# Optimization experiments

Hardware: AMD Instinct MI355X
Metric: run time of the kernel (lower is better)

Reference implementation:

```python
import jax, jax.numpy as jnp
import numpy as np

N = 100000
E = 1200000
IN_DIM, PE_DIM, HID, LAT, K = 48, 16, 64, 32, 4


def setup_inputs() -> dict:
    key = jax.random.key(0)
    ks = jax.random.split(key, 12)
    s = 0.05
    return {
        "x": jax.random.normal(ks[0], (N, IN_DIM), dtype=jnp.float32),
        "edge_index": jax.random.randint(ks[1], (2, E), 0, N, dtype=jnp.int32),
        "lap_pe": jax.random.normal(ks[2], (N, PE_DIM), dtype=jnp.float32),
        "cheb1_W": jax.random.normal(ks[3], (K, IN_DIM + PE_DIM, HID), dtype=jnp.float32) * s,
        "cheb1_b": jnp.zeros((HID,), dtype=jnp.float32),
        "cheb2_W": jax.random.normal(ks[4], (K, HID, HID), dtype=jnp.float32) * s,
        "cheb2_b": jnp.zeros((HID,), dtype=jnp.float32),
        "mu_W": jax.random.normal(ks[5], (HID, LAT), dtype=jnp.float32) * s,
        "mu_b": jnp.zeros((LAT,), dtype=jnp.float32),
        "lv_W": jax.random.normal(ks[6], (HID, LAT), dtype=jnp.float32) * s,
        "lv_b": jnp.zeros((LAT,), dtype=jnp.float32),
    }


def _cheb_norm(edge_index, num_nodes):
    # PyG ChebConv.__norm__ with edge_weight=ones (self-loops added then removed),
    # normalization='sym', lambda_max=2.0. Scaled Laplacian L_hat = L - I has
    # zero diagonal and off-diagonal -D^{-1/2} A D^{-1/2}.
    row, col = edge_index[0], edge_index[1]
    w = jnp.where(row == col, 0.0, 1.0).astype(jnp.float32)  # remove_self_loops
    deg = jax.ops.segment_sum(w, row, num_segments=num_nodes)
    dis = jnp.where(deg > 0, jax.lax.rsqrt(jnp.maximum(deg, 1.0)), 0.0)
    norm = -dis[row] * w * dis[col]  # (2/lambda_max)=1 with lambda_max=2
    return row, col, norm


def _cheb_conv(x, row, col, norm, W, b):
    num_nodes = x.shape[0]

    def prop(h):  # L_hat @ h : gather sources, scale, scatter to targets
        return jax.ops.segment_sum(norm[:, None] * h[row], col, num_segments=num_nodes)

    Tx0 = x
    out = Tx0 @ W[0]
    Tx1 = prop(Tx0)
    out = out + Tx1 @ W[1]
    for k in range(2, W.shape[0]):  # Chebyshev recurrence T_k = 2 L T_{k-1} - T_{k-2}
        Tx2 = 2.0 * prop(Tx1) - Tx0
        out = out + Tx2 @ W[k]
        Tx0, Tx1 = Tx1, Tx2
    return out + b


def reference(x, edge_index, lap_pe, cheb1_W, cheb1_b, cheb2_W, cheb2_b, mu_W, mu_b, lv_W, lv_b):
    num_nodes = x.shape[0]
    xc = jnp.concatenate([x, lap_pe], axis=1)  # [N, in+pe]
    # forward adds self-loops (weight 1) but ChebConv strips them again internally
    row, col, norm = _cheb_norm(edge_index, num_nodes)
    h = jax.nn.relu(_cheb_conv(xc, row, col, norm, cheb1_W, cheb1_b))
    h = jax.nn.relu(_cheb_conv(h, row, col, norm, cheb2_W, cheb2_b))
    graph_embed = jnp.mean(h, axis=0, keepdims=True)  # scatter_mean, batch all-zero -> [1, HID]
    mu = graph_embed @ mu_W + mu_b
    logvar = graph_embed @ lv_W + lv_b
    return mu, logvar
```

## Files before the change

kernel.cpp:

```cpp
#include <hip/hip_runtime.h>


#define WPB 4
#define CAP 48
#define EB  256

typedef unsigned int u32;
typedef unsigned short u16;
typedef __bf16 bf16x8 __attribute__((ext_vector_type(8)));
typedef float f32x4 __attribute__((ext_vector_type(4)));

__device__ __forceinline__ float bf2f(u16 h) { return __uint_as_float(((u32)h) << 16); }
__device__ __forceinline__ u16 f2bf(float f) {
  u32 u = __float_as_uint(f);
  return (u16)((u + 0x7fffu + ((u >> 16) & 1u)) >> 16);
}
__device__ __forceinline__ u32 cvtpk_bf16(float lo, float hi) {
  u32 r;
  asm("v_cvt_pk_bf16_f32 %0, %1, %2" : "=v"(r) : "v"(lo), "v"(hi));
  return r;
}
__device__ __forceinline__ u32 pk_fp8x4(float a, float b, float c, float d) {
  u32 r = __builtin_amdgcn_cvt_pk_fp8_f32(a, b, 0u, false);
  return __builtin_amdgcn_cvt_pk_fp8_f32(c, d, r, true);
}


__global__ void __launch_bounds__(256) k_b1(const int* __restrict__ ei, int E, int EPB,
                                            int NBC, u32* __restrict__ H) {
  __shared__ u32 sh[2048];
  int nbt = 2 * NBC;
  for (int i = threadIdx.x; i < nbt; i += 256) sh[i] = 0;
  __syncthreads();
  int s = blockIdx.x * EPB, e1 = s + EPB;
  if (e1 > E) e1 = E;
  for (int e = s + threadIdx.x; e < e1; e += 256) {
    int r = ei[e], c = ei[E + e];
    if (r == c) continue;
    atomicAdd(&sh[c >> 7], 1u);
    atomicAdd(&sh[NBC + (r >> 7)], 1u);
  }
  __syncthreads();
  for (int i = threadIdx.x; i < nbt; i += 256) H[(size_t)i * EB + blockIdx.x] = sh[i];
}

__global__ void __launch_bounds__(256) k_b2a(const u32* __restrict__ H, u32* __restrict__ P,
                                             u32* __restrict__ S) {
  __shared__ u32 sh[EB];
  int bb = blockIdx.x, tid = threadIdx.x;
  u32 v = H[(size_t)bb * EB + tid];
  sh[tid] = v;
  __syncthreads();
  for (int ofs = 1; ofs < EB; ofs <<= 1) {
    u32 add = (tid >= ofs) ? sh[tid - ofs] : 0;
    __syncthreads();
    sh[tid] += add;
    __syncthreads();
  }
  P[(size_t)bb * EB + tid] = sh[tid] - v;
  if (tid == EB - 1) S[bb] = sh[EB - 1];
}

__global__ void __launch_bounds__(256) k_b3(const int* __restrict__ ei, int E, int EPB,
                                            int NBC, const u32* __restrict__ P,
                                            const u32* __restrict__ S,
                                            u32* __restrict__ BaseOut,
                                            u32* __restrict__ cbuf) {
  __shared__ u32 cur[2048];
  __shared__ u32 sh2[256];
  int nbt = 2 * NBC, tid = threadIdx.x;
  int per = (nbt + 255) / 256;
  u32 loc = 0;
  for (int i = 0; i < per; i++) {
    int idx = tid * per + i;
    if (idx < nbt) loc += S[idx];
  }
  sh2[tid] = loc;
  __syncthreads();
  for (int ofs = 1; ofs < 256; ofs <<= 1) {
    u32 a = (tid >= ofs) ? sh2[tid - ofs] : 0;
    __syncthreads();
    sh2[tid] += a;
    __syncthreads();
  }
  u32 run = sh2[tid] - loc;
  for (int i = 0; i < per; i++) {
    int idx = tid * per + i;
    if (idx < nbt) {
      cur[idx] = run + P[(size_t)idx * EB + blockIdx.x];
      if (blockIdx.x == 0) BaseOut[idx] = run;
      run += S[idx];
    }
  }
  if (blockIdx.x == 0 && tid == 255) BaseOut[nbt] = run;
  __syncthreads();
  int s = blockIdx.x * EPB, e1 = s + EPB;
  if (e1 > E) e1 = E;
  for (int e = s + tid; e < e1; e += 256) {
    int r = ei[e], c = ei[E + e];
    if (r == c) continue;
    u32 p1 = atomicAdd(&cur[c >> 7], 1u);
    cbuf[p1] = ((u32)r << 7) | (u32)(c & 127);
    u32 p2 = atomicAdd(&cur[NBC + (r >> 7)], 1u);
    cbuf[p2] = (u32)(r & 127);
  }
}

__global__ void __launch_bounds__(256) k_b4(const u32* __restrict__ Base, int NBC, int N,
                                            const u32* __restrict__ cbuf,
                                            int* __restrict__ csr, int* __restrict__ cnt,
                                            int* __restrict__ deg) {
  __shared__ u32 h[128];
  int bb = blockIdx.x, tid = threadIdx.x;
  if (tid < 128) h[tid] = 0;
  __syncthreads();
  u32 lo = Base[bb], hi = Base[bb + 1];
  if (bb < NBC) {
    int c0 = bb << 7;
    for (u32 e = lo + tid; e < hi; e += 256) {
      u32 w = cbuf[e];
      int cl = w & 127;
      u32 p = atomicAdd(&h[cl], 1u);
      if (p < CAP) csr[(size_t)(c0 + cl) * CAP + p] = (int)(w >> 7);
    }
    __syncthreads();
    if (tid < 128 && c0 + tid < N) cnt[c0 + tid] = (int)h[tid];
  } else {
    int r0 = (bb - NBC) << 7;
    for (u32 e = lo + tid; e < hi; e += 256) atomicAdd(&h[cbuf[e] & 127], 1u);
    __syncthreads();
    if (tid < 128 && r0 + tid < N) deg[r0 + tid] = (int)h[tid];
  }
}


__global__ void k_dis(const int* __restrict__ deg, float2* __restrict__ dis2, int N) {
  int v = blockIdx.x * blockDim.x + threadIdx.x;
  if (v < N) {
    int d = deg[v];
    float df = (float)d;
    dis2[v] = (d > 0) ? make_float2(rsqrtf(df), sqrtf(df)) : make_float2(0.f, 0.f);
  }
}

__global__ void k_init(const float* __restrict__ W1, const float* __restrict__ W2,
                       u16* __restrict__ Wt1, u16* __restrict__ Wt2,
                       u32* g0, u32* g1, u32* g2, u32* g3, int N) {
  int b = blockIdx.x;
  if (b < 128) {
    const float* W = (b < 64) ? W1 : W2;
    u16* Wt = (b < 64) ? Wt1 : Wt2;
    int i = (b & 63) * 256 + threadIdx.x;
    int k = i >> 6, c = i & 63;
    Wt[c * 256 + k] = f2bf(W[i]);
  } else if (threadIdx.x < 64) {
    int tid = threadIdx.x;
    u32* p = (tid < 16) ? g0 : (tid < 32) ? g1 : (tid < 48) ? g2 : g3;
    p[(size_t)N * 16 + (tid & 15)] = 0;
  }
}

__global__ void __launch_bounds__(256) k_concat(
    const float* __restrict__ x, const float* __restrict__ pe,
    const float2* __restrict__ dis2,
    u16* __restrict__ T0, u32* __restrict__ G0, int N) {
  __shared__ float tl[WPB][64];
  int tid = threadIdx.x, lane = tid & 63, wv = tid >> 6;
  int v = blockIdx.x * WPB + wv;
  if (v >= N) return;
  float t = (lane < 48) ? x[(size_t)v * 48 + lane] : pe[(size_t)v * 16 + (lane - 48)];
  T0[(size_t)v * 64 + lane] = f2bf(t);
  tl[wv][lane] = dis2[v].x * t;
  if (lane < 16) {
    const float* p = &tl[wv][lane * 4];
    G0[(size_t)v * 16 + lane] = pk_fp8x4(p[0], p[1], p[2], p[3]);
  }
}

template <int SUB>
__global__ void __launch_bounds__(256) k_prop(
    const int* __restrict__ cnt, const int* __restrict__ csr,
    const float2* __restrict__ dis2,
    const u32* __restrict__ Gsrc, const u32* __restrict__ Gsub,
    u32* __restrict__ Gdst, int N) {
  int tid = threadIdx.x, lane = tid & 63, wv = tid >> 6;
  int half = lane >> 5, sl = lane & 31;
  int v = (blockIdx.x * WPB + wv) * 2 + half;
  int vc = v < N ? v : N - 1;
  int c = (v < N) ? cnt[vc] : 0;
  if (c > CAP) c = CAP;
  const int* base = csr + (size_t)vc * CAP;
  int u0 = (sl < c) ? base[sl] : N;
  int u1 = N;
  if (c > 32 && sl < 16) {
    int s2 = 32 + sl;
    u1 = (s2 < c) ? base[s2] : N;
  }
  int g = (lane >> 3) & 3, fq = lane & 7;
  int sbase = half << 5;
  float a0 = 0, a1 = 0, a2 = 0, a3 = 0, a4 = 0, a5 = 0, a6 = 0, a7 = 0;
#define PGRP(UU, i) { int u = __shfl(UU, sbase + (((i) << 2) | g)); \
    uint2 q = *(const uint2*)(Gsrc + (size_t)u * 16 + fq * 2); \
    auto l0 = __builtin_amdgcn_cvt_pk_f32_fp8(q.x, false); \
    auto h0 = __builtin_amdgcn_cvt_pk_f32_fp8(q.x, true); \
    auto l1 = __builtin_amdgcn_cvt_pk_f32_fp8(q.y, false); \
    auto h1 = __builtin_amdgcn_cvt_pk_f32_fp8(q.y, true); \
    a0 += l0[0]; a1 += l0[1]; a2 += h0[0]; a3 += h0[1]; \
    a4 += l1[0]; a5 += l1[1]; a6 += h1[0]; a7 += h1[1]; }
  PGRP(u0, 0) PGRP(u0, 1) PGRP(u0, 2) PGRP(u0, 3)
  if (c > 16) { PGRP(u0, 4) PGRP(u0, 5) PGRP(u0, 6) PGRP(u0, 7) }
  if (c > 32) { PGRP(u1, 0) PGRP(u1, 1) PGRP(u1, 2) PGRP(u1, 3) }
#undef PGRP
  a0 += __shfl_xor(a0, 8); a0 += __shfl_xor(a0, 16);
  a1 += __shfl_xor(a1, 8); a1 += __shfl_xor(a1, 16);
  a2 += __shfl_xor(a2, 8); a2 += __shfl_xor(a2, 16);
  a3 += __shfl_xor(a3, 8); a3 += __shfl_xor(a3, 16);
  a4 += __shfl_xor(a4, 8); a4 += __shfl_xor(a4, 16);
  a5 += __shfl_xor(a5, 8); a5 += __shfl_xor(a5, 16);
  a6 += __shfl_xor(a6, 8); a6 += __shfl_xor(a6, 16);
  a7 += __shfl_xor(a7, 8); a7 += __shfl_xor(a7, 16);
  if (sl < 8 && v < N) {
    float2 dd = dis2[v];
    float t0 = -dd.x * a0, t1 = -dd.x * a1, t2 = -dd.x * a2, t3 = -dd.x * a3;
    float t4 = -dd.x * a4, t5 = -dd.x * a5, t6 = -dd.x * a6, t7 = -dd.x * a7;
    if (SUB) {
      uint2 sq = *(const uint2*)(Gsub + (size_t)v * 16 + fq * 2);
      auto l0 = __builtin_amdgcn_cvt_pk_f32_fp8(sq.x, false);
      auto h0 = __builtin_amdgcn_cvt_pk_f32_fp8(sq.x, true);
      auto l1 = __builtin_amdgcn_cvt_pk_f32_fp8(sq.y, false);
      auto h1 = __builtin_amdgcn_cvt_pk_f32_fp8(sq.y, true);
      t0 = 2.f * t0 - dd.y * l0[0];
      t1 = 2.f * t1 - dd.y * l0[1];
      t2 = 2.f * t2 - dd.y * h0[0];
      t3 = 2.f * t3 - dd.y * h0[1];
      t4 = 2.f * t4 - dd.y * l1[0];
      t5 = 2.f * t5 - dd.y * l1[1];
      t6 = 2.f * t6 - dd.y * h1[0];
      t7 = 2.f * t7 - dd.y * h1[1];
    }
    uint2 o;
    o.x = pk_fp8x4(dd.x * t0, dd.x * t1, dd.x * t2, dd.x * t3);
    o.y = pk_fp8x4(dd.x * t4, dd.x * t5, dd.x * t6, dd.x * t7);
    *(uint2*)(Gdst + (size_t)v * 16 + fq * 2) = o;
  }
}

__device__ __forceinline__ bf16x8 fp8_frag(const u32* rp, float s) {
  u32 q0 = rp[0], q1 = rp[1];
  auto a = __builtin_amdgcn_cvt_pk_f32_fp8(q0, false);
  auto b = __builtin_amdgcn_cvt_pk_f32_fp8(q0, true);
  auto c = __builtin_amdgcn_cvt_pk_f32_fp8(q1, false);
  auto d = __builtin_amdgcn_cvt_pk_f32_fp8(q1, true);
  union { u32 q[4]; bf16x8 v; } r;
  r.q[0] = cvtpk_bf16(a[0] * s, a[1] * s);
  r.q[1] = cvtpk_bf16(b[0] * s, b[1] * s);
  r.q[2] = cvtpk_bf16(c[0] * s, c[1] * s);
  r.q[3] = cvtpk_bf16(d[0] * s, d[1] * s);
  return r.v;
}

template <int EPI>
__global__ void __launch_bounds__(256) k_gemm(
    const u16* __restrict__ T, const u32* __restrict__ G0,
    const u32* __restrict__ G1, const u32* __restrict__ G2,
    const u32* __restrict__ G3,
    const u16* __restrict__ Wt, const float* __restrict__ bias,
    const float2* __restrict__ dis2,
    u32* __restrict__ outG, float* __restrict__ gm, int N) {
  __shared__ float smem[EPI ? 256 : 4 * 16 * 65];
  int tid = threadIdx.x, lane = tid & 63, wv = tid >> 6;
  int r0 = blockIdx.x * 64 + wv * 16;
  int fr = lane & 15, kg = lane >> 4;
  int arow = r0 + fr;
  if (arow > N - 1) arow = N - 1;
  float dvi = dis2[arow].y;
  f32x4 acc[4] = {};
  const u16* wb = Wt + (size_t)fr * 256 + kg * 8;
  const u32* gbuf[4] = {G0, G1, G2, G3};
#pragma unroll
  for (int s = 0; s < 8; ++s) {
    bf16x8 a;
    if (EPI == 0 && s < 2)
      a = *(const bf16x8*)(T + (size_t)arow * 64 + s * 32 + kg * 8);
    else
      a = fp8_frag(gbuf[s >> 1] + (size_t)arow * 16 + (s & 1) * 8 + kg * 2, dvi);
#pragma unroll
    for (int cc = 0; cc < 4; ++cc) {
      bf16x8 b = *(const bf16x8*)(wb + (size_t)cc * 16 * 256 + s * 32);
      acc[cc] = __builtin_amdgcn_mfma_f32_16x16x32_bf16(a, b, acc[cc], 0, 0, 0);
    }
  }
  if (EPI == 0) {
    float* hl = smem + wv * 16 * 65;
#pragma unroll
    for (int reg = 0; reg < 4; ++reg) {
#pragma unroll
      for (int cc = 0; cc < 4; ++cc) {
        float vv = acc[cc][reg] + bias[cc * 16 + fr];
        hl[(kg * 4 + reg) * 65 + cc * 16 + fr] = vv > 0.f ? vv : 0.f;
      }
    }
    int rr = lane >> 2, dg = lane & 3;
    int grow = r0 + rr;
    if (grow < N) {
      float ds = dis2[grow].x;
      const float* hp = hl + rr * 65 + dg * 16;
      uint4 o;
      o.x = pk_fp8x4(ds * hp[0], ds * hp[1], ds * hp[2], ds * hp[3]);
      o.y = pk_fp8x4(ds * hp[4], ds * hp[5], ds * hp[6], ds * hp[7]);
      o.z = pk_fp8x4(ds * hp[8], ds * hp[9], ds * hp[10], ds * hp[11]);
      o.w = pk_fp8x4(ds * hp[12], ds * hp[13], ds * hp[14], ds * hp[15]);
      *(uint4*)(outG + (size_t)grow * 16 + dg * 4) = o;
    }
  } else {
    float pc[4] = {0.f, 0.f, 0.f, 0.f};
#pragma unroll
    for (int reg = 0; reg < 4; ++reg) {
      int row = r0 + kg * 4 + reg;
      if (row < N) {
#pragma unroll
        for (int cc = 0; cc < 4; ++cc) {
          float vv = acc[cc][reg] + bias[cc * 16 + fr];
          pc[cc] += (vv > 0.f ? vv : 0.f);
        }
      }
    }
#pragma unroll
    for (int cc = 0; cc < 4; ++cc) {
      pc[cc] += __shfl_xor(pc[cc], 16);
      pc[cc] += __shfl_xor(pc[cc], 32);
    }
    if (lane < 16) {
#pragma unroll
      for (int cc = 0; cc < 4; ++cc) smem[wv * 64 + cc * 16 + lane] = pc[cc];
    }
    __syncthreads();
    if (tid < 64)
      atomicAdd(&gm[(blockIdx.x & 63) * 64 + tid],
                smem[tid] + smem[64 + tid] + smem[128 + tid] + smem[192 + tid]);
  }
}

__global__ void k_head(const float* __restrict__ gm, int N,
                       const float* __restrict__ muW, const float* __restrict__ mub,
                       const float* __restrict__ lvW, const float* __restrict__ lvb,
                       float* __restrict__ outp) {
  __shared__ float gs[64];
  int j = threadIdx.x;
  if (j < 64) {
    float s = 0.f;
    for (int k = 0; k < 64; ++k) s += gm[k * 64 + j];
    gs[j] = s;
  }
  __syncthreads();
  if (j < 64) {
    const float* W = (j < 32) ? muW : lvW;
    const float* b = (j < 32) ? mub : lvb;
    int jj = j & 31;
    float invN = 1.0f / (float)N;
    float acc = 0.0f;
    for (int f = 0; f < 64; f++) acc = fmaf(gs[f] * invN, W[f * 32 + jj], acc);
    outp[j] = acc + b[jj];
  }
}

extern "C" void kernel_launch(void* const* d_in, const int* in_sizes, int n_in,
                              void* d_out, int out_size, void* d_ws, size_t ws_size,
                              hipStream_t stream) {
  const float* x   = (const float*)d_in[0];
  const int*   ei  = (const int*)d_in[1];
  const float* pe  = (const float*)d_in[2];
  const float* W1  = (const float*)d_in[3];
  const float* b1  = (const float*)d_in[4];
  const float* W2  = (const float*)d_in[5];
  const float* b2  = (const float*)d_in[6];
  const float* muW = (const float*)d_in[7];
  const float* mub = (const float*)d_in[8];
  const float* lvW = (const float*)d_in[9];
  const float* lvb = (const float*)d_in[10];
  const int N = in_sizes[0] / 48;
  const int E = in_sizes[1] / 2;
  const int NBC = (N + 127) >> 7;
  const int NBT = 2 * NBC;
  const int EPB = (E + EB - 1) / EB;

  char* ws = (char*)d_ws;
  size_t off = 0;
  auto take = [&](size_t bytes) -> char* {
    char* p = ws + off;
    off = (off + bytes + 255) & ~(size_t)255;
    return p;
  };
  const size_t GSZ = (size_t)(N + 1) * 64;
  int*    deg    = (int*)take((size_t)N * 4);
  float2* dis2   = (float2*)take((size_t)N * 8);
  int*    cnt    = (int*)take((size_t)N * 4);
  int*    csr    = (int*)take((size_t)N * CAP * 4);
  u32*    Hh     = (u32*)take((size_t)NBT * EB * 4);
  u32*    Pp     = (u32*)take((size_t)NBT * EB * 4);
  u32*    Ss     = (u32*)take((size_t)NBT * 4);
  u32*    Base   = (u32*)take((size_t)(NBT + 1) * 4);
  u32*    cbuf   = (u32*)take((size_t)2 * E * 4);
  u16*    T0     = (u16*)take((size_t)N * 64 * 2);
  u32*    G0     = (u32*)take(GSZ);
  u32*    G1     = (u32*)take(GSZ);
  u32*    G2     = (u32*)take(GSZ);
  u32*    G3     = (u32*)take(GSZ);
  u16*    Wt1    = (u16*)take(256 * 64 * 2);
  u16*    Wt2    = (u16*)take(256 * 64 * 2);
  float*  gm     = (float*)take(64 * 64 * 4);

  hipMemsetAsync(gm, 0, 64 * 64 * 4, stream);

  int nb = (N + 255) / 256;
  k_init<<<129, 256, 0, stream>>>(W1, W2, Wt1, Wt2, G0, G1, G2, G3, N);
  k_b1<<<EB, 256, 0, stream>>>(ei, E, EPB, NBC, Hh);
  k_b2a<<<NBT, 256, 0, stream>>>(Hh, Pp, Ss);
  k_b3<<<EB, 256, 0, stream>>>(ei, E, EPB, NBC, Pp, Ss, Base, cbuf);
  k_b4<<<NBT, 256, 0, stream>>>(Base, NBC, N, cbuf, csr, cnt, deg);
  k_dis<<<nb, 256, 0, stream>>>(deg, dis2, N);

  int vb = (N + WPB - 1) / WPB;
  int pb = (N + 2 * WPB - 1) / (2 * WPB);
  int gb = (N + 63) / 64;
  k_concat<<<vb, 256, 0, stream>>>(x, pe, dis2, T0, G0, N);
  k_prop<0><<<pb, 256, 0, stream>>>(cnt, csr, dis2, G0, nullptr, G1, N);
  k_prop<1><<<pb, 256, 0, stream>>>(cnt, csr, dis2, G1, G0, G2, N);
  k_prop<1><<<pb, 256, 0, stream>>>(cnt, csr, dis2, G2, G1, G3, N);
  k_gemm<0><<<gb, 256, 0, stream>>>(T0, G0, G1, G2, G3, Wt1, b1, dis2, G0, nullptr, N);
  k_prop<0><<<pb, 256, 0, stream>>>(cnt, csr, dis2, G0, nullptr, G1, N);
  k_prop<1><<<pb, 256, 0, stream>>>(cnt, csr, dis2, G1, G0, G2, N);
  k_prop<1><<<pb, 256, 0, stream>>>(cnt, csr, dis2, G2, G1, G3, N);
  k_gemm<1><<<gb, 256, 0, stream>>>(nullptr, G0, G1, G2, G3, Wt2, b2, dis2, nullptr, gm, N);
  k_head<<<1, 64, 0, stream>>>(gm, N, muW, mub, lvW, lvb, (float*)d_out);
}
```

Baseline: 271.2 us.

## Fold init and dis kernels into CSR build, widen prop to 16B gathers

Merges the weight-transpose/init kernel into k_b1 as extra blocks and computes dis2 directly in k_b4, removing two kernel launches and the deg buffer round trip. The propagation kernel now handles four nodes per wave with 16 lanes each, loading 16-byte fp8 rows per lane and reducing across fewer shuffle steps. This is meant to cut launch overhead and improve gather efficiency in the memory-bound prop kernels. In exchange, each lane holds 16 accumulators, which raises register pressure.

```diff
diff --git a/kernel.cpp b/kernel.cpp
--- a/kernel.cpp
+++ b/kernel.cpp
@@ -27,7 +27,26 @@
 
 
 __global__ void __launch_bounds__(256) k_b1(const int* __restrict__ ei, int E, int EPB,
-                                            int NBC, u32* __restrict__ H) {
+                                            int NBC, u32* __restrict__ H,
+                                            const float* __restrict__ W1,
+                                            const float* __restrict__ W2,
+                                            u16* __restrict__ Wt1, u16* __restrict__ Wt2,
+                                            u32* g0, u32* g1, u32* g2, u32* g3, int N) {
+  if (blockIdx.x >= EB) {
+    int b = blockIdx.x - EB;
+    if (b < 128) {
+      const float* W = (b < 64) ? W1 : W2;
+      u16* Wt = (b < 64) ? Wt1 : Wt2;
+      int i = (b & 63) * 256 + threadIdx.x;
+      int k = i >> 6, c = i & 63;
+      Wt[c * 256 + k] = f2bf(W[i]);
+    } else if (threadIdx.x < 64) {
+      int tid = threadIdx.x;
+      u32* p = (tid < 16) ? g0 : (tid < 32) ? g1 : (tid < 48) ? g2 : g3;
+      p[(size_t)N * 16 + (tid & 15)] = 0;
+    }
+    return;
+  }
   __shared__ u32 sh[2048];
   int nbt = 2 * NBC;
   for (int i = threadIdx.x; i < nbt; i += 256) sh[i] = 0;
@@ -109,7 +128,7 @@
 __global__ void __launch_bounds__(256) k_b4(const u32* __restrict__ Base, int NBC, int N,
                                             const u32* __restrict__ cbuf,
                                             int* __restrict__ csr, int* __restrict__ cnt,
-                                            int* __restrict__ deg) {
+                                            float2* __restrict__ dis2) {
   __shared__ u32 h[128];
   int bb = blockIdx.x, tid = threadIdx.x;
   if (tid < 128) h[tid] = 0;
@@ -129,36 +148,14 @@
     int r0 = (bb - NBC) << 7;
     for (u32 e = lo + tid; e < hi; e += 256) atomicAdd(&h[cbuf[e] & 127], 1u);
     __syncthreads();
-    if (tid < 128 && r0 + tid < N) deg[r0 + tid] = (int)h[tid];
-  }
-}
-
-
-__global__ void k_dis(const int* __restrict__ deg, float2* __restrict__ dis2, int N) {
-  int v = blockIdx.x * blockDim.x + threadIdx.x;
-  if (v < N) {
-    int d = deg[v];
-    float df = (float)d;
-    dis2[v] = (d > 0) ? make_float2(rsqrtf(df), sqrtf(df)) : make_float2(0.f, 0.f);
-  }
-}
-
-__global__ void k_init(const float* __restrict__ W1, const float* __restrict__ W2,
-                       u16* __restrict__ Wt1, u16* __restrict__ Wt2,
-                       u32* g0, u32* g1, u32* g2, u32* g3, int N) {
-  int b = blockIdx.x;
-  if (b < 128) {
-    const float* W = (b < 64) ? W1 : W2;
-    u16* Wt = (b < 64) ? Wt1 : Wt2;
-    int i = (b & 63) * 256 + threadIdx.x;
-    int k = i >> 6, c = i & 63;
-    Wt[c * 256 + k] = f2bf(W[i]);
-  } else if (threadIdx.x < 64) {
-    int tid = threadIdx.x;
-    u32* p = (tid < 16) ? g0 : (tid < 32) ? g1 : (tid < 48) ? g2 : g3;
-    p[(size_t)N * 16 + (tid & 15)] = 0;
-  }
-}
+    if (tid < 128 && r0 + tid < N) {
+      int d = (int)h[tid];
+      float df = (float)d;
+      dis2[r0 + tid] = (d > 0) ? make_float2(rsqrtf(df), sqrtf(df)) : make_float2(0.f, 0.f);
+    }
+  }
+}
+
 
 __global__ void __launch_bounds__(256) k_concat(
     const float* __restrict__ x, const float* __restrict__ pe,
@@ -184,64 +181,73 @@
     const u32* __restrict__ Gsrc, const u32* __restrict__ Gsub,
     u32* __restrict__ Gdst, int N) {
   int tid = threadIdx.x, lane = tid & 63, wv = tid >> 6;
-  int half = lane >> 5, sl = lane & 31;
-  int v = (blockIdx.x * WPB + wv) * 2 + half;
+  int q = lane >> 4, sl = lane & 15;
+  int v = (blockIdx.x * WPB + wv) * 4 + q;
   int vc = v < N ? v : N - 1;
   int c = (v < N) ? cnt[vc] : 0;
   if (c > CAP) c = CAP;
   const int* base = csr + (size_t)vc * CAP;
   int u0 = (sl < c) ? base[sl] : N;
-  int u1 = N;
-  if (c > 32 && sl < 16) {
-    int s2 = 32 + sl;
-    u1 = (s2 < c) ? base[s2] : N;
-  }
-  int g = (lane >> 3) & 3, fq = lane & 7;
-  int sbase = half << 5;
+  int u1 = N, u2 = N;
+  if (c > 16) { int s2 = 16 + sl; u1 = (s2 < c) ? base[s2] : N; }
+  if (c > 32) { int s3 = 32 + sl; u2 = (s3 < c) ? base[s3] : N; }
+  int qb = lane & 48;
+  int eg = (lane >> 2) & 3, fo = lane & 3;
   float a0 = 0, a1 = 0, a2 = 0, a3 = 0, a4 = 0, a5 = 0, a6 = 0, a7 = 0;
-#define PGRP(UU, i) { int u = __shfl(UU, sbase + (((i) << 2) | g)); \
-    uint2 q = *(const uint2*)(Gsrc + (size_t)u * 16 + fq * 2); \
-    auto l0 = __builtin_amdgcn_cvt_pk_f32_fp8(q.x, false); \
-    auto h0 = __builtin_amdgcn_cvt_pk_f32_fp8(q.x, true); \
-    auto l1 = __builtin_amdgcn_cvt_pk_f32_fp8(q.y, false); \
-    auto h1 = __builtin_amdgcn_cvt_pk_f32_fp8(q.y, true); \
-    a0 += l0[0]; a1 += l0[1]; a2 += h0[0]; a3 += h0[1]; \
-    a4 += l1[0]; a5 += l1[1]; a6 += h1[0]; a7 += h1[1]; }
+  float a8 = 0, a9 = 0, a10 = 0, a11 = 0, a12 = 0, a13 = 0, a14 = 0, a15 = 0;
+#define PGRP(UU, i) { int u = __shfl(UU, qb + (((i) << 2) | eg)); \
+    uint4 qq = *(const uint4*)(Gsrc + (size_t)u * 16 + fo * 4); \
+    auto p0 = __builtin_amdgcn_cvt_pk_f32_fp8(qq.x, false); \
+    auto p1 = __builtin_amdgcn_cvt_pk_f32_fp8(qq.x, true); \
+    auto p2 = __builtin_amdgcn_cvt_pk_f32_fp8(qq.y, false); \
+    auto p3 = __builtin_amdgcn_cvt_pk_f32_fp8(qq.y, true); \
+    auto p4 = __builtin_amdgcn_cvt_pk_f32_fp8(qq.z, false); \
+    auto p5 = __builtin_amdgcn_cvt_pk_f32_fp8(qq.z, true); \
+    auto p6 = __builtin_amdgcn_cvt_pk_f32_fp8(qq.w, false); \
+    auto p7 = __builtin_amdgcn_cvt_pk_f32_fp8(qq.w, true); \
+    a0 += p0[0]; a1 += p0[1]; a2 += p1[0]; a3 += p1[1]; \
+    a4 += p2[0]; a5 += p2[1]; a6 += p3[0]; a7 += p3[1]; \
+    a8 += p4[0]; a9 += p4[1]; a10 += p5[0]; a11 += p5[1]; \
+    a12 += p6[0]; a13 += p6[1]; a14 += p7[0]; a15 += p7[1]; }
   PGRP(u0, 0) PGRP(u0, 1) PGRP(u0, 2) PGRP(u0, 3)
-  if (c > 16) { PGRP(u0, 4) PGRP(u0, 5) PGRP(u0, 6) PGRP(u0, 7) }
-  if (c > 32) { PGRP(u1, 0) PGRP(u1, 1) PGRP(u1, 2) PGRP(u1, 3) }
+  if (c > 16) { PGRP(u1, 0) PGRP(u1, 1) PGRP(u1, 2) PGRP(u1, 3) }
+  if (c > 32) { PGRP(u2, 0) PGRP(u2, 1) PGRP(u2, 2) PGRP(u2, 3) }
 #undef PGRP
-  a0 += __shfl_xor(a0, 8); a0 += __shfl_xor(a0, 16);
-  a1 += __shfl_xor(a1, 8); a1 += __shfl_xor(a1, 16);
-  a2 += __shfl_xor(a2, 8); a2 += __shfl_xor(a2, 16);
-  a3 += __shfl_xor(a3, 8); a3 += __shfl_xor(a3, 16);
-  a4 += __shfl_xor(a4, 8); a4 += __shfl_xor(a4, 16);
-  a5 += __shfl_xor(a5, 8); a5 += __shfl_xor(a5, 16);
-  a6 += __shfl_xor(a6, 8); a6 += __shfl_xor(a6, 16);
-  a7 += __shfl_xor(a7, 8); a7 += __shfl_xor(a7, 16);
-  if (sl < 8 && v < N) {
+#define FOLD(A) A += __shfl_xor(A, 4); A += __shfl_xor(A, 8);
+  FOLD(a0) FOLD(a1) FOLD(a2) FOLD(a3) FOLD(a4) FOLD(a5) FOLD(a6) FOLD(a7)
+  FOLD(a8) FOLD(a9) FOLD(a10) FOLD(a11) FOLD(a12) FOLD(a13) FOLD(a14) FOLD(a15)
+#undef FOLD
+  if (eg == 0 && v < N) {
     float2 dd = dis2[v];
     float t0 = -dd.x * a0, t1 = -dd.x * a1, t2 = -dd.x * a2, t3 = -dd.x * a3;
     float t4 = -dd.x * a4, t5 = -dd.x * a5, t6 = -dd.x * a6, t7 = -dd.x * a7;
+    float t8 = -dd.x * a8, t9 = -dd.x * a9, t10 = -dd.x * a10, t11 = -dd.x * a11;
+    float t12 = -dd.x * a12, t13 = -dd.x * a13, t14 = -dd.x * a14, t15 = -dd.x * a15;
     if (SUB) {
-      uint2 sq = *(const uint2*)(Gsub + (size_t)v * 16 + fq * 2);
-      auto l0 = __builtin_amdgcn_cvt_pk_f32_fp8(sq.x, false);
-      auto h0 = __builtin_amdgcn_cvt_pk_f32_fp8(sq.x, true);
-      auto l1 = __builtin_amdgcn_cvt_pk_f32_fp8(sq.y, false);
-      auto h1 = __builtin_amdgcn_cvt_pk_f32_fp8(sq.y, true);
-      t0 = 2.f * t0 - dd.y * l0[0];
-      t1 = 2.f * t1 - dd.y * l0[1];
-      t2 = 2.f * t2 - dd.y * h0[0];
-      t3 = 2.f * t3 - dd.y * h0[1];
-      t4 = 2.f * t4 - dd.y * l1[0];
-      t5 = 2.f * t5 - dd.y * l1[1];
-      t6 = 2.f * t6 - dd.y * h1[0];
-      t7 = 2.f * t7 - dd.y * h1[1];
-    }
-    uint2 o;
+      uint4 sq = *(const uint4*)(Gsub + (size_t)v * 16 + fo * 4);
+      auto s0 = __builtin_amdgcn_cvt_pk_f32_fp8(sq.x, false);
+      auto s1 = __builtin_amdgcn_cvt_pk_f32_fp8(sq.x, true);
+      auto s2 = __builtin_amdgcn_cvt_pk_f32_fp8(sq.y, false);
+      auto s3 = __builtin_amdgcn_cvt_pk_f32_fp8(sq.y, true);
+      auto s4 = __builtin_amdgcn_cvt_pk_f32_fp8(sq.z, false);
+      auto s5 = __builtin_amdgcn_cvt_pk_f32_fp8(sq.z, true);
+      auto s6 = __builtin_amdgcn_cvt_pk_f32_fp8(sq.w, false);
+      auto s7 = __builtin_amdgcn_cvt_pk_f32_fp8(sq.w, true);
+      t0 = 2.f * t0 - dd.y * s0[0];  t1 = 2.f * t1 - dd.y * s0[1];
+      t2 = 2.f * t2 - dd.y * s1[0];  t3 = 2.f * t3 - dd.y * s1[1];
+      t4 = 2.f * t4 - dd.y * s2[0];  t5 = 2.f * t5 - dd.y * s2[1];
+      t6 = 2.f * t6 - dd.y * s3[0];  t7 = 2.f * t7 - dd.y * s3[1];
+      t8 = 2.f * t8 - dd.y * s4[0];  t9 = 2.f * t9 - dd.y * s4[1];
+      t10 = 2.f * t10 - dd.y * s5[0]; t11 = 2.f * t11 - dd.y * s5[1];
+      t12 = 2.f * t12 - dd.y * s6[0]; t13 = 2.f * t13 - dd.y * s6[1];
+      t14 = 2.f * t14 - dd.y * s7[0]; t15 = 2.f * t15 - dd.y * s7[1];
+    }
+    uint4 o;
     o.x = pk_fp8x4(dd.x * t0, dd.x * t1, dd.x * t2, dd.x * t3);
     o.y = pk_fp8x4(dd.x * t4, dd.x * t5, dd.x * t6, dd.x * t7);
-    *(uint2*)(Gdst + (size_t)v * 16 + fq * 2) = o;
+    o.z = pk_fp8x4(dd.x * t8, dd.x * t9, dd.x * t10, dd.x * t11);
+    o.w = pk_fp8x4(dd.x * t12, dd.x * t13, dd.x * t14, dd.x * t15);
+    *(uint4*)(Gdst + (size_t)v * 16 + fo * 4) = o;
   }
 }
 
@@ -392,7 +398,6 @@
     return p;
   };
   const size_t GSZ = (size_t)(N + 1) * 64;
-  int*    deg    = (int*)take((size_t)N * 4);
   float2* dis2   = (float2*)take((size_t)N * 8);
   int*    cnt    = (int*)take((size_t)N * 4);
   int*    csr    = (int*)take((size_t)N * CAP * 4);
@@ -412,16 +417,14 @@
 
   hipMemsetAsync(gm, 0, 64 * 64 * 4, stream);
 
-  int nb = (N + 255) / 256;
-  k_init<<<129, 256, 0, stream>>>(W1, W2, Wt1, Wt2, G0, G1, G2, G3, N);
-  k_b1<<<EB, 256, 0, stream>>>(ei, E, EPB, NBC, Hh);
+  k_b1<<<EB + 129, 256, 0, stream>>>(ei, E, EPB, NBC, Hh, W1, W2, Wt1, Wt2,
+                                     G0, G1, G2, G3, N);
   k_b2a<<<NBT, 256, 0, stream>>>(Hh, Pp, Ss);
   k_b3<<<EB, 256, 0, stream>>>(ei, E, EPB, NBC, Pp, Ss, Base, cbuf);
-  k_b4<<<NBT, 256, 0, stream>>>(Base, NBC, N, cbuf, csr, cnt, deg);
-  k_dis<<<nb, 256, 0, stream>>>(deg, dis2, N);
+  k_b4<<<NBT, 256, 0, stream>>>(Base, NBC, N, cbuf, csr, cnt, dis2);
 
   int vb = (N + WPB - 1) / WPB;
-  int pb = (N + 2 * WPB - 1) / (2 * WPB);
+  int pb = (N + 4 * WPB - 1) / (4 * WPB);
   int gb = (N + 63) / 64;
   k_concat<<<vb, 256, 0, stream>>>(x, pe, dis2, T0, G0, N);
   k_prop<0><<<pb, 256, 0, stream>>>(cnt, csr, dis2, G0, nullptr, G1, N);
```

Result: no change. 268.5 us (-1.0%).
